# Kernel tuning notes

Hardware: AMD Instinct MI355X
Metric: run time of the kernel (lower is better)

The kernel has to match this reference:

```python
import jax, jax.numpy as jnp
import numpy as np

N = 50000
E = 800000
NUM_GRAPHS = 64
D_IN = 261
D_SAGE = 64
D_LIN = 32
N_SAGE_REST = 6
N_LIN_REST = 3
EPS = 1e-5


def _layernorm(x, g, b):
    mu = jnp.mean(x, axis=-1, keepdims=True)
    var = jnp.mean((x - mu) ** 2, axis=-1, keepdims=True)
    return (x - mu) * jax.lax.rsqrt(var + EPS) * g + b


def _sage_block(x, Wl, bl, Wr, g, b, src, dst, inv_deg, residual):
    # mean aggregation of neighbor (source) features onto targets
    msum = jax.ops.segment_sum(x[src], dst, num_segments=N)  # [N, d]
    mean = msum * inv_deg  # [N, d]
    f = mean @ Wl + bl + x @ Wr  # lin_l(aggr) + lin_r(x); lin_r has no bias
    f = jax.nn.gelu(f, approximate=False)
    f = _layernorm(f, g, b)
    if residual:
        f = f + x
    return f


def _lin_block(x, W, b, g, beta, residual):
    f = jax.nn.gelu(x @ W + b, approximate=False)
    f = _layernorm(f, g, beta)
    if residual:
        f = f + x
    return f


def setup_inputs() -> dict:
    key = jax.random.key(0)
    ks = jax.random.split(key, 24)
    x = jax.random.normal(ks[0], (N, D_IN), dtype=jnp.float32)
    edge_index = jax.random.randint(ks[1], (2, E), 0, N, dtype=jnp.int64)
    batch = jnp.sort(jax.random.randint(ks[2], (N,), 0, NUM_GRAPHS, dtype=jnp.int64))

    def glorot(k, shape):
        fan_in = shape[0]
        return jax.random.normal(k, shape, dtype=jnp.float32) / np.sqrt(fan_in)

    inp = {
        "x": x, "edge_index": edge_index, "batch": batch,
        # first SAGE block (261 -> 64, no residual)
        "Wl0": glorot(ks[3], (D_IN, D_SAGE)), "bl0": jnp.zeros((D_SAGE,), jnp.float32),
        "Wr0": glorot(ks[4], (D_IN, D_SAGE)),
        "g0": jnp.ones((D_SAGE,), jnp.float32), "beta0": jnp.zeros((D_SAGE,), jnp.float32),
        # 6 residual SAGE blocks (64 -> 64), stacked
        "Wl": glorot(ks[5], (N_SAGE_REST, D_SAGE, D_SAGE)),
        "bl": jnp.zeros((N_SAGE_REST, D_SAGE), jnp.float32),
        "Wr": glorot(ks[6], (N_SAGE_REST, D_SAGE, D_SAGE)),
        "g": jnp.ones((N_SAGE_REST, D_SAGE), jnp.float32),
        "beta": jnp.zeros((N_SAGE_REST, D_SAGE), jnp.float32),
        # MLP: first LinearBlock 64 -> 32 (no residual)
        "M0": glorot(ks[7], (D_SAGE, D_LIN)), "mb0": jnp.zeros((D_LIN,), jnp.float32),
        "mg0": jnp.ones((D_LIN,), jnp.float32), "mbeta0": jnp.zeros((D_LIN,), jnp.float32),
        # 3 residual LinearBlocks 32 -> 32, stacked
        "M": glorot(ks[8], (N_LIN_REST, D_LIN, D_LIN)),
        "mb": jnp.zeros((N_LIN_REST, D_LIN), jnp.float32),
        "mg": jnp.ones((N_LIN_REST, D_LIN), jnp.float32),
        "mbeta": jnp.zeros((N_LIN_REST, D_LIN), jnp.float32),
        # final Linear 32 -> 1
        "Wf": glorot(ks[9], (D_LIN, 1)), "bf": jnp.zeros((1,), jnp.float32),
    }
    return inp


def reference(x, edge_index, batch, Wl0, bl0, Wr0, g0, beta0, Wl, bl, Wr, g, beta,
              M0, mb0, mg0, mbeta0, M, mb, mg, mbeta, Wf, bf):
    src, dst = edge_index[0], edge_index[1]
    deg = jax.ops.segment_sum(jnp.ones((E,), x.dtype), dst, num_segments=N)
    inv_deg = (1.0 / jnp.maximum(deg, 1.0))[:, None]  # [N,1]

    h = _sage_block(x, Wl0, bl0, Wr0, g0, beta0, src, dst, inv_deg, residual=False)
    for i in range(N_SAGE_REST):
        h = _sage_block(h, Wl[i], bl[i], Wr[i], g[i], beta[i], src, dst, inv_deg, residual=True)

    pooled = jax.ops.segment_sum(h, batch, num_segments=NUM_GRAPHS)  # [G, 64]

    m = _lin_block(pooled, M0, mb0, mg0, mbeta0, residual=False)
    for i in range(N_LIN_REST):
        m = _lin_block(m, M[i], mb[i], mg[i], mbeta[i], residual=True)
    return m @ Wf + bf  # [G, 1]
```

## Files before the change

### kernel.cpp

```cpp
#include <hip/hip_runtime.h>
#include <hip/hip_bf16.h>
#include <math.h>

#define N_NODES 50000
#define N_EDGES 800000
#define NUM_GRAPHS 64
#define NPAD 50048
#define KPAD0 288
#define PSPLIT 16
#define MAXDEG 64

#define G0_GRID    (NPAD / 32)
#define LAYER_GRID (NPAD / 32)
#define PREPW_TOT  (128 * KPAD0 + 6 * 128 * 64)
#define PREPW_GRID ((PREPW_TOT + 255) / 256)
#define CONV_GRID  (NPAD * (KPAD0 / 8) / 256)

#define SLICES 8
#define NPS 6250
#define SCHUNK 2048
#define SCHUNKS ((N_EDGES + SCHUNK - 1) / SCHUNK)
#define SCAT_GRID (SCHUNKS * SLICES)
#define FRONT_GRID (SCAT_GRID + CONV_GRID + PREPW_GRID)

typedef __attribute__((ext_vector_type(8))) short short8;
typedef __attribute__((ext_vector_type(4))) float f32x4;

__device__ __forceinline__ float gelu_f(float v) {
    return 0.5f * v * (1.0f + erff(v * 0.70710678118654752440f));
}

__device__ __forceinline__ float half_sum32(float v) {
    v += __shfl_xor(v, 1); v += __shfl_xor(v, 2); v += __shfl_xor(v, 4);
    v += __shfl_xor(v, 8); v += __shfl_xor(v, 16);
    return v;
}

__device__ __forceinline__ float group_sum8(float v) {
    v += __shfl_xor(v, 1); v += __shfl_xor(v, 2); v += __shfl_xor(v, 4);
    return v;
}

__device__ __forceinline__ unsigned short f2bf(float f) {
    unsigned int u = __float_as_uint(f);
    unsigned int r = (u + 0x7fffu + ((u >> 16) & 1u)) >> 16;
    return (unsigned short)r;
}

__device__ __forceinline__ float bf_lo(unsigned int u) {
    return __uint_as_float(u << 16);
}
__device__ __forceinline__ float bf_hi(unsigned int u) {
    return __uint_as_float(u & 0xffff0000u);
}


__global__ __launch_bounds__(256) void k_front(
        const int* __restrict__ src, const int* __restrict__ dst,
        int* __restrict__ deg, unsigned short* __restrict__ col64,
        const float* __restrict__ X, unsigned short* __restrict__ Xbf,
        const float* __restrict__ Wl0, const float* __restrict__ Wr0,
        const float* __restrict__ Wl, const float* __restrict__ Wr,
        unsigned short* __restrict__ Bt0, unsigned short* __restrict__ BtR) {
    const int blk = blockIdx.x;
    const int tid = threadIdx.x;
    if (blk < SCAT_GRID) {
        const int s = blk & (SLICES - 1);
        const int c = blk >> 3;
        const int base = c * SCHUNK;
        const int lim = min(base + SCHUNK, N_EDGES);
        for (int i = base + tid; i < lim; i += 256) {
            int d = dst[i];
            if (d / NPS == s) {
                int sv = src[i];
                int pos = atomicAdd(&deg[d], 1);
                if (pos < MAXDEG) col64[(d << 6) + pos] = (unsigned short)sv;
            }
        }
        return;
    }
    if (blk < SCAT_GRID + CONV_GRID) {
        int t = (blk - SCAT_GRID) * 256 + tid;
        int node = t / (KPAD0 / 8);
        int k8 = (t - node * (KPAD0 / 8)) * 8;
        short8 v8;
        if (node < N_NODES) {
            #pragma unroll
            for (int j = 0; j < 8; ++j) {
                int k = k8 + j;
                float val = (k < 261) ? X[(size_t)node * 261 + k] : 0.0f;
                v8[j] = (short)f2bf(val);
            }
        } else {
            #pragma unroll
            for (int j = 0; j < 8; ++j) v8[j] = 0;
        }
        *(short8*)&Xbf[(size_t)node * KPAD0 + k8] = v8;
        return;
    }
    int idx = (blk - SCAT_GRID - CONV_GRID) * 256 + tid;
    const int n0 = 128 * KPAD0;
    if (idx < n0) {
        int j = idx / KPAD0, k = idx - j * KPAD0;
        float v = 0.0f;
        if (k < 261) v = (j < 64) ? Wl0[k * 64 + j] : Wr0[k * 64 + (j - 64)];
        Bt0[idx] = f2bf(v);
    } else if (idx < PREPW_TOT) {
        int r = idx - n0;
        int l = r >> 13;
        int rr = r & 8191;
        int j = rr >> 6, k = rr & 63;
        float v = (j < 64) ? Wl[l * 4096 + k * 64 + j] : Wr[l * 4096 + k * 64 + (j - 64)];
        BtR[r] = f2bf(v);
    }
}


__global__ __launch_bounds__(256) void k_gemm0(
        const unsigned short* __restrict__ Xbf, const unsigned short* __restrict__ Bt0,
        unsigned short* __restrict__ U, float* __restrict__ V) {
    __shared__ __align__(16) unsigned short sB[64 * 296];
    const int tid = threadIdx.x;
    const int lane = tid & 63, wid = tid >> 6;
    const int l16 = lane & 15, quad = lane >> 4;
    const int ch = blockIdx.x & 1;
    const int m0 = (blockIdx.x >> 1) * 64;
    #pragma unroll
    for (int k = 0; k < 9; ++k) {
        int g = k * 256 + tid;
        int row = g / 36;
        int part = (g - row * 36) * 8;
        *(short8*)&sB[row * 296 + part] =
            *(const short8*)&Bt0[(size_t)(ch * 64 + row) * KPAD0 + part];
    }
    f32x4 acc[4];
    #pragma unroll
    for (int j = 0; j < 4; ++j) { acc[j][0] = 0.f; acc[j][1] = 0.f; acc[j][2] = 0.f; acc[j][3] = 0.f; }
    const unsigned short* xr = Xbf + (size_t)(m0 + wid * 16 + l16) * KPAD0 + quad * 8;
    __syncthreads();
    for (int kc = 0; kc < KPAD0; kc += 32) {
        short8 af = *(const short8*)(xr + kc);
        #pragma unroll
        for (int j = 0; j < 4; ++j) {
            short8 bfv = *(const short8*)&sB[(j * 16 + l16) * 296 + kc + quad * 8];
            acc[j] = __builtin_amdgcn_mfma_f32_16x16x32_bf16(af, bfv, acc[j], 0, 0, 0);
        }
    }
    const int rbase = m0 + wid * 16 + quad * 4;
    if (ch == 0) {
        #pragma unroll
        for (int j = 0; j < 4; ++j)
            #pragma unroll
            for (int r = 0; r < 4; ++r)
                U[(size_t)(rbase + r) * 64 + j * 16 + l16] = f2bf(acc[j][r]);
    } else {
        #pragma unroll
        for (int j = 0; j < 4; ++j)
            #pragma unroll
            for (int r = 0; r < 4; ++r)
                V[(size_t)(rbase + r) * 64 + j * 16 + l16] = acc[j][r];
    }
}


__global__ __launch_bounds__(256) void k_layer(
        const unsigned short* __restrict__ U_in, const float* __restrict__ V_in,
        unsigned short* __restrict__ h,
        const int* __restrict__ deg, const unsigned short* __restrict__ col64,
        const float* __restrict__ bias, const float* __restrict__ gam,
        const float* __restrict__ bet,
        const unsigned short* __restrict__ Bt_next,
        unsigned short* __restrict__ U_out, float* __restrict__ V_out,
        const int* __restrict__ batch, float* __restrict__ pool_part,
        int residual, int have_gemm) {
    __shared__ __align__(16) unsigned short sA[2 * 32 * 32];
    __shared__ __align__(16) unsigned short sB[128 * 72];
    const int tid = threadIdx.x;
    const int lane = tid & 63, wid = tid >> 6;
    const int sub = lane >> 3, hl = lane & 7;
    const int base = lane & 56;
    const int m0 = blockIdx.x * 32;
    const uint4* __restrict__ Up = (const uint4*)U_in;

    if (have_gemm) {
        #pragma unroll
        for (int k = 0; k < 4; ++k) {
            int g = k * 256 + tid;
            int row = g >> 3, part = (g & 7) * 8;
            *(short8*)&sB[row * 72 + part] = *(const short8*)&Bt_next[(size_t)row * 64 + part];
        }
    }

    const int nl = wid * 8 + sub;
    const int node = m0 + nl;
    const bool valid = (node < N_NODES);
    const int nd = valid ? node : 0;
    const int dg = valid ? deg[nd] : 0;
    const int cnt = min(dg, MAXDEG);
    uint4 cv = make_uint4(0u, 0u, 0u, 0u);
    if (valid) cv = *(const uint4*)&col64[((size_t)nd << 6) + hl * 8];
    float s0 = 0.f, s1 = 0.f, s2 = 0.f, s3 = 0.f, s4 = 0.f, s5 = 0.f, s6 = 0.f, s7 = 0.f;
    for (int b = 0; b * 8 < cnt; b += 2) {
        #pragma unroll
        for (int hh = 0; hh < 2; ++hh) {
            const int sl = base + b + hh;
            unsigned int p0 = (unsigned int)__shfl((int)cv.x, sl);
            unsigned int p1 = (unsigned int)__shfl((int)cv.y, sl);
            unsigned int p2 = (unsigned int)__shfl((int)cv.z, sl);
            unsigned int p3 = (unsigned int)__shfl((int)cv.w, sl);
            const int eb = (b + hh) * 8;
            int c[8];
            c[0] = (int)(p0 & 0xffffu); c[1] = (int)(p0 >> 16);
            c[2] = (int)(p1 & 0xffffu); c[3] = (int)(p1 >> 16);
            c[4] = (int)(p2 & 0xffffu); c[5] = (int)(p2 >> 16);
            c[6] = (int)(p3 & 0xffffu); c[7] = (int)(p3 >> 16);
            #pragma unroll
            for (int i = 0; i < 8; ++i) {
                uint4 u = (eb + i < cnt) ? Up[(size_t)c[i] * 8 + hl] : make_uint4(0u, 0u, 0u, 0u);
                s0 += bf_lo(u.x); s1 += bf_hi(u.x);
                s2 += bf_lo(u.y); s3 += bf_hi(u.y);
                s4 += bf_lo(u.z); s5 += bf_hi(u.z);
                s6 += bf_lo(u.w); s7 += bf_hi(u.w);
            }
        }
    }
    const float id = 1.0f / fmaxf((float)dg, 1.0f);
    const float4 b0 = *(const float4*)&bias[8 * hl];
    const float4 b1 = *(const float4*)&bias[8 * hl + 4];
    float4 v0 = make_float4(0.f, 0.f, 0.f, 0.f), v1 = v0;
    if (valid) {
        v0 = *(const float4*)&V_in[(size_t)nd * 64 + 8 * hl];
        v1 = *(const float4*)&V_in[(size_t)nd * 64 + 8 * hl + 4];
    }
    float f0 = gelu_f(s0 * id + b0.x + v0.x);
    float f1 = gelu_f(s1 * id + b0.y + v0.y);
    float f2 = gelu_f(s2 * id + b0.z + v0.z);
    float f3 = gelu_f(s3 * id + b0.w + v0.w);
    float f4 = gelu_f(s4 * id + b1.x + v1.x);
    float f5 = gelu_f(s5 * id + b1.y + v1.y);
    float f6 = gelu_f(s6 * id + b1.z + v1.z);
    float f7 = gelu_f(s7 * id + b1.w + v1.w);
    float mu = group_sum8(((f0 + f1) + (f2 + f3)) + ((f4 + f5) + (f6 + f7))) * 0.015625f;
    float d0 = f0 - mu, d1 = f1 - mu, d2 = f2 - mu, d3 = f3 - mu;
    float d4 = f4 - mu, d5 = f5 - mu, d6 = f6 - mu, d7 = f7 - mu;
    float var = group_sum8(((d0 * d0 + d1 * d1) + (d2 * d2 + d3 * d3)) +
                           ((d4 * d4 + d5 * d5) + (d6 * d6 + d7 * d7))) * 0.015625f;
    float rs = rsqrtf(var + 1e-5f);
    const float4 g0v = *(const float4*)&gam[8 * hl];
    const float4 g1v = *(const float4*)&gam[8 * hl + 4];
    const float4 e0v = *(const float4*)&bet[8 * hl];
    const float4 e1v = *(const float4*)&bet[8 * hl + 4];
    f0 = d0 * rs * g0v.x + e0v.x;
    f1 = d1 * rs * g0v.y + e0v.y;
    f2 = d2 * rs * g0v.z + e0v.z;
    f3 = d3 * rs * g0v.w + e0v.w;
    f4 = d4 * rs * g1v.x + e1v.x;
    f5 = d5 * rs * g1v.y + e1v.y;
    f6 = d6 * rs * g1v.z + e1v.z;
    f7 = d7 * rs * g1v.w + e1v.w;
    if (residual && valid) {
        uint4 hu = ((const uint4*)h)[(size_t)nd * 8 + hl];
        f0 += bf_lo(hu.x); f1 += bf_hi(hu.x);
        f2 += bf_lo(hu.y); f3 += bf_hi(hu.y);
        f4 += bf_lo(hu.z); f5 += bf_hi(hu.z);
        f6 += bf_lo(hu.w); f7 += bf_hi(hu.w);
    }

    if (pool_part) {
        const int myg = valid ? batch[nd] : -1;
        const int i_lo = (m0 < N_NODES) ? m0 : (N_NODES - 1);
        const int i_hi = (m0 + 31 < N_NODES) ? (m0 + 31) : (N_NODES - 1);
        const int g_lo = batch[i_lo];
        const int g_hi = batch[i_hi];
        const int split = blockIdx.x & (PSPLIT - 1);
        for (int g = g_lo; g <= g_hi; ++g) {
            const bool mine = (myg == g);
            float p0 = mine ? f0 : 0.f, p1 = mine ? f1 : 0.f;
            float p2 = mine ? f2 : 0.f, p3 = mine ? f3 : 0.f;
            float p4 = mine ? f4 : 0.f, p5 = mine ? f5 : 0.f;
            float p6 = mine ? f6 : 0.f, p7 = mine ? f7 : 0.f;
            p0 += __shfl_xor(p0, 8);  p1 += __shfl_xor(p1, 8);
            p2 += __shfl_xor(p2, 8);  p3 += __shfl_xor(p3, 8);
            p4 += __shfl_xor(p4, 8);  p5 += __shfl_xor(p5, 8);
            p6 += __shfl_xor(p6, 8);  p7 += __shfl_xor(p7, 8);
            p0 += __shfl_xor(p0, 16); p1 += __shfl_xor(p1, 16);
            p2 += __shfl_xor(p2, 16); p3 += __shfl_xor(p3, 16);
            p4 += __shfl_xor(p4, 16); p5 += __shfl_xor(p5, 16);
            p6 += __shfl_xor(p6, 16); p7 += __shfl_xor(p7, 16);
            p0 += __shfl_xor(p0, 32); p1 += __shfl_xor(p1, 32);
            p2 += __shfl_xor(p2, 32); p3 += __shfl_xor(p3, 32);
            p4 += __shfl_xor(p4, 32); p5 += __shfl_xor(p5, 32);
            p6 += __shfl_xor(p6, 32); p7 += __shfl_xor(p7, 32);
            if (sub == 0) {
                float* dp = &pool_part[((size_t)g * PSPLIT + split) * 64 + 8 * hl];
                atomicAdd(dp + 0, p0); atomicAdd(dp + 1, p1);
                atomicAdd(dp + 2, p2); atomicAdd(dp + 3, p3);
                atomicAdd(dp + 4, p4); atomicAdd(dp + 5, p5);
                atomicAdd(dp + 6, p6); atomicAdd(dp + 7, p7);
            }
        }
        return;
    }

    uint4 outw;
    outw.x = (unsigned int)f2bf(f0) | ((unsigned int)f2bf(f1) << 16);
    outw.y = (unsigned int)f2bf(f2) | ((unsigned int)f2bf(f3) << 16);
    outw.z = (unsigned int)f2bf(f4) | ((unsigned int)f2bf(f5) << 16);
    outw.w = (unsigned int)f2bf(f6) | ((unsigned int)f2bf(f7) << 16);
    if (valid) ((uint4*)h)[(size_t)nd * 8 + hl] = outw;
    *(uint4*)&sA[(((hl >> 2) * 32 + nl) << 5) + (hl & 3) * 8] = outw;

    if (!have_gemm) return;
    __syncthreads();

    const int l16 = lane & 15, quad = lane >> 4;
    const int wrow = wid & 1, colh = wid >> 1;
    f32x4 acc[4];
    #pragma unroll
    for (int j = 0; j < 4; ++j) { acc[j][0] = 0.f; acc[j][1] = 0.f; acc[j][2] = 0.f; acc[j][3] = 0.f; }
    #pragma unroll
    for (int kc = 0; kc < 64; kc += 32) {
        short8 af = *(const short8*)&sA[(((kc >> 5) * 32 + wrow * 16 + l16) << 5) + quad * 8];
        #pragma unroll
        for (int j = 0; j < 4; ++j) {
            short8 bfv = *(const short8*)&sB[(colh * 64 + j * 16 + l16) * 72 + kc + quad * 8];
            acc[j] = __builtin_amdgcn_mfma_f32_16x16x32_bf16(af, bfv, acc[j], 0, 0, 0);
        }
    }
    const int rbase = m0 + wrow * 16 + quad * 4;
    if (colh == 0) {
        #pragma unroll
        for (int j = 0; j < 4; ++j)
            #pragma unroll
            for (int r = 0; r < 4; ++r)
                U_out[(size_t)(rbase + r) * 64 + j * 16 + l16] = f2bf(acc[j][r]);
    } else {
        #pragma unroll
        for (int j = 0; j < 4; ++j)
            #pragma unroll
            for (int r = 0; r < 4; ++r)
                V_out[(size_t)(rbase + r) * 64 + j * 16 + l16] = acc[j][r];
    }
}


__global__ __launch_bounds__(1024) void k_head(const float* __restrict__ partial,
                                               const float* __restrict__ M0, const float* __restrict__ mb0,
                                               const float* __restrict__ mg0, const float* __restrict__ mbeta0,
                                               const float* __restrict__ M, const float* __restrict__ mb,
                                               const float* __restrict__ mg, const float* __restrict__ mbeta,
                                               const float* __restrict__ Wf, const float* __restrict__ bf,
                                               float* __restrict__ out) {
    __shared__ float sP[64 * 64];
    __shared__ float sA[64 * 33];
    __shared__ float sB[64 * 33];
    const int tx = threadIdx.x, ty = threadIdx.y;
    const int tid = ty * 32 + tx;
    for (int i = tid; i < 64 * 64; i += 1024) {
        int g = i >> 6, f = i & 63;
        float s = 0.0f;
        #pragma unroll
        for (int s2 = 0; s2 < PSPLIT; ++s2) s += partial[(size_t)(g * PSPLIT + s2) * 64 + f];
        sP[i] = s;
    }
    __syncthreads();
    #pragma unroll
    for (int rr = 0; rr < 2; ++rr) {
        int r = ty + rr * 32;
        float a = mb0[tx];
        for (int k = 0; k < 64; ++k) a += sP[r * 64 + k] * M0[k * 32 + tx];
        a = gelu_f(a);
        float mu = half_sum32(a) * (1.0f / 32.0f);
        float d = a - mu;
        float var = half_sum32(d * d) * (1.0f / 32.0f);
        a = d * rsqrtf(var + 1e-5f) * mg0[tx] + mbeta0[tx];
        sA[r * 33 + tx] = a;
    }
    __syncthreads();
    float* cur = sA;
    float* nxt = sB;
    for (int L = 0; L < 3; ++L) {
        const float* Mi = M + L * 32 * 32;
        const float* mbi = mb + L * 32;
        const float* mgi = mg + L * 32;
        const float* mbetai = mbeta + L * 32;
        #pragma unroll
        for (int rr = 0; rr < 2; ++rr) {
            int r = ty + rr * 32;
            float a = mbi[tx];
            for (int k = 0; k < 32; ++k) a += cur[r * 33 + k] * Mi[k * 32 + tx];
            a = gelu_f(a);
            float mu = half_sum32(a) * (1.0f / 32.0f);
            float d = a - mu;
            float var = half_sum32(d * d) * (1.0f / 32.0f);
            a = d * rsqrtf(var + 1e-5f) * mgi[tx] + mbetai[tx] + cur[r * 33 + tx];
            nxt[r * 33 + tx] = a;
        }
        __syncthreads();
        float* t = cur; cur = nxt; nxt = t;
    }
    #pragma unroll
    for (int rr = 0; rr < 2; ++rr) {
        int r = ty + rr * 32;
        float p = cur[r * 33 + tx] * Wf[tx];
        p = half_sum32(p);
        if (tx == 0) out[r] = p + bf[0];
    }
}


extern "C" void kernel_launch(void* const* d_in, const int* in_sizes, int n_in,
                              void* d_out, int out_size, void* d_ws, size_t ws_size,
                              hipStream_t stream) {
    const int N = N_NODES;
    const int E = N_EDGES;

    const float* x    = (const float*)d_in[0];
    const int* eidx   = (const int*)d_in[1];
    const int* batch  = (const int*)d_in[2];
    const float* Wl0  = (const float*)d_in[3];
    const float* bl0  = (const float*)d_in[4];
    const float* Wr0  = (const float*)d_in[5];
    const float* g0   = (const float*)d_in[6];
    const float* bet0 = (const float*)d_in[7];
    const float* Wl   = (const float*)d_in[8];
    const float* bl   = (const float*)d_in[9];
    const float* Wr   = (const float*)d_in[10];
    const float* gR   = (const float*)d_in[11];
    const float* betR = (const float*)d_in[12];
    const float* M0   = (const float*)d_in[13];
    const float* mb0  = (const float*)d_in[14];
    const float* mg0  = (const float*)d_in[15];
    const float* mbe0 = (const float*)d_in[16];
    const float* M    = (const float*)d_in[17];
    const float* mb   = (const float*)d_in[18];
    const float* mg   = (const float*)d_in[19];
    const float* mbe  = (const float*)d_in[20];
    const float* Wf   = (const float*)d_in[21];
    const float* bf   = (const float*)d_in[22];

    const int* src = eidx;
    const int* dst = eidx + E;

    char* p = (char*)d_ws;
    auto alloc = [&](size_t bytes) -> void* {
        void* q = (void*)p;
        p += (bytes + 255) & ~(size_t)255;
        return q;
    };
    int*   deg     = (int*)alloc((size_t)N * 4);
    float* partial = (float*)alloc((size_t)NUM_GRAPHS * PSPLIT * 64 * 4);
    unsigned short* col64 = (unsigned short*)alloc((size_t)N * MAXDEG * 2);
    unsigned short* Bt0 = (unsigned short*)alloc((size_t)128 * KPAD0 * 2);
    unsigned short* BtR = (unsigned short*)alloc((size_t)6 * 128 * 64 * 2);
    unsigned short* Xbf = (unsigned short*)alloc((size_t)NPAD * KPAD0 * 2);
    unsigned short* Ua  = (unsigned short*)alloc((size_t)NPAD * 64 * 2);
    unsigned short* Ub  = (unsigned short*)alloc((size_t)NPAD * 64 * 2);
    float* Va   = (float*)alloc((size_t)NPAD * 64 * 4);
    float* Vb   = (float*)alloc((size_t)NPAD * 64 * 4);
    unsigned short* hbuf = (unsigned short*)alloc((size_t)NPAD * 64 * 2);

    size_t zspan = (size_t)((char*)col64 - (char*)deg);
    hipMemsetAsync(deg, 0, zspan, stream);

    k_front<<<FRONT_GRID, 256, 0, stream>>>(
        src, dst, deg, col64, x, Xbf, Wl0, Wr0, Wl, Wr, Bt0, BtR);

    k_gemm0<<<G0_GRID, 256, 0, stream>>>(Xbf, Bt0, Ua, Va);

    unsigned short* Uin = Ua;  float* Vin = Va;
    unsigned short* Uout = Ub; float* Vout = Vb;
    for (int i = 0; i < 7; ++i) {
        const float* bias = (i == 0) ? bl0  : bl  + (size_t)(i - 1) * 64;
        const float* gam  = (i == 0) ? g0   : gR  + (size_t)(i - 1) * 64;
        const float* bet  = (i == 0) ? bet0 : betR + (size_t)(i - 1) * 64;
        const int have_gemm = (i < 6);
        float* pool_part = (i == 6) ? partial : nullptr;
        k_layer<<<LAYER_GRID, 256, 0, stream>>>(
            Uin, Vin, hbuf, deg, col64, bias, gam, bet,
            have_gemm ? (BtR + (size_t)i * 128 * 64) : BtR,
            Uout, Vout, batch, pool_part, (i > 0) ? 1 : 0, have_gemm);
        unsigned short* tu = Uin; Uin = Uout; Uout = tu;
        float* tv = Vin; Vin = Vout; Vout = tv;
    }

    k_head<<<1, dim3(32, 32), 0, stream>>>(partial, M0, mb0, mg0, mbe0, M, mb, mg, mbe, Wf, bf, (float*)d_out);
}
```

Before: 381.9 us.

## Co-schedule edge scatter with first-layer GEMM in an interleaved kernel

Moves the edge-to-CSR scatter out of the front prep kernel and interleaves its blocks with the first GEMM blocks inside one kernel (two scatter blocks per GEMM block), launched as two halves. The aim is to overlap the atomic-heavy, latency-bound scatter with the compute-bound MFMA GEMM so both share the GPU. It also adds nontemporal loads on X, src and dst to reduce cache pollution. This adds one more kernel launch and makes the scatter depend on finishing the conversion kernel first. The GEMM is still correct, since the prep kernel that produces Xbf runs beforehand.

```diff
diff --git a/kernel.cpp b/kernel.cpp
--- a/kernel.cpp
+++ b/kernel.cpp
@@ -10,18 +10,21 @@
 #define PSPLIT 16
 #define MAXDEG 64
 
-#define G0_GRID    (NPAD / 32)
 #define LAYER_GRID (NPAD / 32)
 #define PREPW_TOT  (128 * KPAD0 + 6 * 128 * 64)
 #define PREPW_GRID ((PREPW_TOT + 255) / 256)
 #define CONV_GRID  (NPAD * (KPAD0 / 8) / 256)
+#define PREP2_GRID (CONV_GRID + PREPW_GRID)
 
 #define SLICES 8
 #define NPS 6250
 #define SCHUNK 2048
 #define SCHUNKS ((N_EDGES + SCHUNK - 1) / SCHUNK)
 #define SCAT_GRID (SCHUNKS * SLICES)
-#define FRONT_GRID (SCAT_GRID + CONV_GRID + PREPW_GRID)
+
+#define MID_TRIPLES 1564
+#define MID_GRID (MID_TRIPLES * 3)
+#define MID_HALF (MID_GRID / 2)
 
 typedef __attribute__((ext_vector_type(8))) short short8;
 typedef __attribute__((ext_vector_type(4))) float f32x4;
@@ -55,32 +58,15 @@
 }
 
 
-__global__ __launch_bounds__(256) void k_front(
-        const int* __restrict__ src, const int* __restrict__ dst,
-        int* __restrict__ deg, unsigned short* __restrict__ col64,
+__global__ __launch_bounds__(256) void k_prep2(
         const float* __restrict__ X, unsigned short* __restrict__ Xbf,
         const float* __restrict__ Wl0, const float* __restrict__ Wr0,
         const float* __restrict__ Wl, const float* __restrict__ Wr,
         unsigned short* __restrict__ Bt0, unsigned short* __restrict__ BtR) {
     const int blk = blockIdx.x;
     const int tid = threadIdx.x;
-    if (blk < SCAT_GRID) {
-        const int s = blk & (SLICES - 1);
-        const int c = blk >> 3;
-        const int base = c * SCHUNK;
-        const int lim = min(base + SCHUNK, N_EDGES);
-        for (int i = base + tid; i < lim; i += 256) {
-            int d = dst[i];
-            if (d / NPS == s) {
-                int sv = src[i];
-                int pos = atomicAdd(&deg[d], 1);
-                if (pos < MAXDEG) col64[(d << 6) + pos] = (unsigned short)sv;
-            }
-        }
-        return;
-    }
-    if (blk < SCAT_GRID + CONV_GRID) {
-        int t = (blk - SCAT_GRID) * 256 + tid;
+    if (blk < CONV_GRID) {
+        int t = blk * 256 + tid;
         int node = t / (KPAD0 / 8);
         int k8 = (t - node * (KPAD0 / 8)) * 8;
         short8 v8;
@@ -88,7 +74,7 @@
             #pragma unroll
             for (int j = 0; j < 8; ++j) {
                 int k = k8 + j;
-                float val = (k < 261) ? X[(size_t)node * 261 + k] : 0.0f;
+                float val = (k < 261) ? __builtin_nontemporal_load(&X[(size_t)node * 261 + k]) : 0.0f;
                 v8[j] = (short)f2bf(val);
             }
         } else {
@@ -98,7 +84,7 @@
         *(short8*)&Xbf[(size_t)node * KPAD0 + k8] = v8;
         return;
     }
-    int idx = (blk - SCAT_GRID - CONV_GRID) * 256 + tid;
+    int idx = (blk - CONV_GRID) * 256 + tid;
     const int n0 = 128 * KPAD0;
     if (idx < n0) {
         int j = idx / KPAD0, k = idx - j * KPAD0;
@@ -116,20 +102,42 @@
 }
 
 
-__global__ __launch_bounds__(256) void k_gemm0(
+__global__ __launch_bounds__(256) void k_mid(
+        int offset,
+        const int* __restrict__ src, const int* __restrict__ dst,
+        int* __restrict__ deg, unsigned short* __restrict__ col64,
         const unsigned short* __restrict__ Xbf, const unsigned short* __restrict__ Bt0,
         unsigned short* __restrict__ U, float* __restrict__ V) {
     __shared__ __align__(16) unsigned short sB[64 * 296];
+    const int blk = blockIdx.x + offset;
     const int tid = threadIdx.x;
+    const int g = blk / 3;
+    const int r = blk - g * 3;
+    if (r < 2) {
+        const int sid = g * 2 + r;
+        const int s = sid & (SLICES - 1);
+        const int c = sid >> 3;
+        const int base = c * SCHUNK;
+        const int lim = min(base + SCHUNK, N_EDGES);
+        for (int i = base + tid; i < lim; i += 256) {
+            int d = __builtin_nontemporal_load(&dst[i]);
+            if (d / NPS == s) {
+                int sv = __builtin_nontemporal_load(&src[i]);
+                int pos = atomicAdd(&deg[d], 1);
+                if (pos < MAXDEG) col64[(d << 6) + pos] = (unsigned short)sv;
+            }
+        }
+        return;
+    }
     const int lane = tid & 63, wid = tid >> 6;
     const int l16 = lane & 15, quad = lane >> 4;
-    const int ch = blockIdx.x & 1;
-    const int m0 = (blockIdx.x >> 1) * 64;
+    const int ch = g & 1;
+    const int m0 = (g >> 1) * 64;
     #pragma unroll
     for (int k = 0; k < 9; ++k) {
-        int g = k * 256 + tid;
-        int row = g / 36;
-        int part = (g - row * 36) * 8;
+        int gg = k * 256 + tid;
+        int row = gg / 36;
+        int part = (gg - row * 36) * 8;
         *(short8*)&sB[row * 296 + part] =
             *(const short8*)&Bt0[(size_t)(ch * 64 + row) * KPAD0 + part];
     }
@@ -151,14 +159,14 @@
         #pragma unroll
         for (int j = 0; j < 4; ++j)
             #pragma unroll
-            for (int r = 0; r < 4; ++r)
-                U[(size_t)(rbase + r) * 64 + j * 16 + l16] = f2bf(acc[j][r]);
+            for (int rr2 = 0; rr2 < 4; ++rr2)
+                U[(size_t)(rbase + rr2) * 64 + j * 16 + l16] = f2bf(acc[j][rr2]);
     } else {
         #pragma unroll
         for (int j = 0; j < 4; ++j)
             #pragma unroll
-            for (int r = 0; r < 4; ++r)
-                V[(size_t)(rbase + r) * 64 + j * 16 + l16] = acc[j][r];
+            for (int rr2 = 0; rr2 < 4; ++rr2)
+                V[(size_t)(rbase + rr2) * 64 + j * 16 + l16] = acc[j][rr2];
     }
 }
 
@@ -463,10 +471,10 @@
     size_t zspan = (size_t)((char*)col64 - (char*)deg);
     hipMemsetAsync(deg, 0, zspan, stream);
 
-    k_front<<<FRONT_GRID, 256, 0, stream>>>(
-        src, dst, deg, col64, x, Xbf, Wl0, Wr0, Wl, Wr, Bt0, BtR);
-
-    k_gemm0<<<G0_GRID, 256, 0, stream>>>(Xbf, Bt0, Ua, Va);
+    k_prep2<<<PREP2_GRID, 256, 0, stream>>>(x, Xbf, Wl0, Wr0, Wl, Wr, Bt0, BtR);
+
+    k_mid<<<MID_HALF, 256, 0, stream>>>(0, src, dst, deg, col64, Xbf, Bt0, Ua, Va);
+    k_mid<<<MID_HALF, 256, 0, stream>>>(MID_HALF, src, dst, deg, col64, Xbf, Bt0, Ua, Va);
 
     unsigned short* Uin = Ua;  float* Vin = Va;
     unsigned short* Uout = Ub; float* Vout = Vb;
```

Result: slower. 436.1 us (+14.2%).

## Split front kernel into prep and two scatter launches, nontemporal loads, hoist loads

Applied to the files above, without the earlier changes.

Splits the fused front kernel into a separate X/weight conversion kernel and an edge-scatter kernel. The scatter is launched as two halves, and dst/src/X reads now use nontemporal loads. In the layer kernel, the V_in and residual h loads are moved ahead of the neighbor-gather loop so their latency overlaps with the gather. The extra launches add overhead, and the streaming-load hints may or may not help the atomic scatter.

```diff
diff --git a/kernel.cpp b/kernel.cpp
--- a/kernel.cpp
+++ b/kernel.cpp
@@ -15,13 +15,13 @@
 #define PREPW_TOT  (128 * KPAD0 + 6 * 128 * 64)
 #define PREPW_GRID ((PREPW_TOT + 255) / 256)
 #define CONV_GRID  (NPAD * (KPAD0 / 8) / 256)
+#define PREP2_GRID (CONV_GRID + PREPW_GRID)
 
 #define SLICES 8
 #define NPS 6250
 #define SCHUNK 2048
 #define SCHUNKS ((N_EDGES + SCHUNK - 1) / SCHUNK)
-#define SCAT_GRID (SCHUNKS * SLICES)
-#define FRONT_GRID (SCAT_GRID + CONV_GRID + PREPW_GRID)
+#define SCAT_SPLIT 196
 
 typedef __attribute__((ext_vector_type(8))) short short8;
 typedef __attribute__((ext_vector_type(4))) float f32x4;
@@ -55,32 +55,15 @@
 }
 
 
-__global__ __launch_bounds__(256) void k_front(
-        const int* __restrict__ src, const int* __restrict__ dst,
-        int* __restrict__ deg, unsigned short* __restrict__ col64,
+__global__ __launch_bounds__(256) void k_prep2(
         const float* __restrict__ X, unsigned short* __restrict__ Xbf,
         const float* __restrict__ Wl0, const float* __restrict__ Wr0,
         const float* __restrict__ Wl, const float* __restrict__ Wr,
         unsigned short* __restrict__ Bt0, unsigned short* __restrict__ BtR) {
     const int blk = blockIdx.x;
     const int tid = threadIdx.x;
-    if (blk < SCAT_GRID) {
-        const int s = blk & (SLICES - 1);
-        const int c = blk >> 3;
-        const int base = c * SCHUNK;
-        const int lim = min(base + SCHUNK, N_EDGES);
-        for (int i = base + tid; i < lim; i += 256) {
-            int d = dst[i];
-            if (d / NPS == s) {
-                int sv = src[i];
-                int pos = atomicAdd(&deg[d], 1);
-                if (pos < MAXDEG) col64[(d << 6) + pos] = (unsigned short)sv;
-            }
-        }
-        return;
-    }
-    if (blk < SCAT_GRID + CONV_GRID) {
-        int t = (blk - SCAT_GRID) * 256 + tid;
+    if (blk < CONV_GRID) {
+        int t = blk * 256 + tid;
         int node = t / (KPAD0 / 8);
         int k8 = (t - node * (KPAD0 / 8)) * 8;
         short8 v8;
@@ -88,7 +71,7 @@
             #pragma unroll
             for (int j = 0; j < 8; ++j) {
                 int k = k8 + j;
-                float val = (k < 261) ? X[(size_t)node * 261 + k] : 0.0f;
+                float val = (k < 261) ? __builtin_nontemporal_load(&X[(size_t)node * 261 + k]) : 0.0f;
                 v8[j] = (short)f2bf(val);
             }
         } else {
@@ -98,7 +81,7 @@
         *(short8*)&Xbf[(size_t)node * KPAD0 + k8] = v8;
         return;
     }
-    int idx = (blk - SCAT_GRID - CONV_GRID) * 256 + tid;
+    int idx = (blk - CONV_GRID) * 256 + tid;
     const int n0 = 128 * KPAD0;
     if (idx < n0) {
         int j = idx / KPAD0, k = idx - j * KPAD0;
@@ -112,6 +95,26 @@
         int j = rr >> 6, k = rr & 63;
         float v = (j < 64) ? Wl[l * 4096 + k * 64 + j] : Wr[l * 4096 + k * 64 + (j - 64)];
         BtR[r] = f2bf(v);
+    }
+}
+
+
+__global__ __launch_bounds__(256) void k_scat(
+        int cbase,
+        const int* __restrict__ src, const int* __restrict__ dst,
+        int* __restrict__ deg, unsigned short* __restrict__ col64) {
+    const int sid = cbase * 8 + blockIdx.x;
+    const int s = sid & (SLICES - 1);
+    const int c = sid >> 3;
+    const int base = c * SCHUNK;
+    const int lim = min(base + SCHUNK, N_EDGES);
+    for (int i = base + (int)threadIdx.x; i < lim; i += 256) {
+        int d = __builtin_nontemporal_load(&dst[i]);
+        if (d / NPS == s) {
+            int sv = __builtin_nontemporal_load(&src[i]);
+            int pos = atomicAdd(&deg[d], 1);
+            if (pos < MAXDEG) col64[(d << 6) + pos] = (unsigned short)sv;
+        }
     }
 }
 
@@ -199,6 +202,15 @@
     const int cnt = min(dg, MAXDEG);
     uint4 cv = make_uint4(0u, 0u, 0u, 0u);
     if (valid) cv = *(const uint4*)&col64[((size_t)nd << 6) + hl * 8];
+
+    float4 v0 = make_float4(0.f, 0.f, 0.f, 0.f), v1 = v0;
+    if (valid) {
+        v0 = *(const float4*)&V_in[(size_t)nd * 64 + 8 * hl];
+        v1 = *(const float4*)&V_in[(size_t)nd * 64 + 8 * hl + 4];
+    }
+    uint4 hu = make_uint4(0u, 0u, 0u, 0u);
+    if (residual && valid) hu = ((const uint4*)h)[(size_t)nd * 8 + hl];
+
     float s0 = 0.f, s1 = 0.f, s2 = 0.f, s3 = 0.f, s4 = 0.f, s5 = 0.f, s6 = 0.f, s7 = 0.f;
     for (int b = 0; b * 8 < cnt; b += 2) {
         #pragma unroll
@@ -227,11 +239,6 @@
     const float id = 1.0f / fmaxf((float)dg, 1.0f);
     const float4 b0 = *(const float4*)&bias[8 * hl];
     const float4 b1 = *(const float4*)&bias[8 * hl + 4];
-    float4 v0 = make_float4(0.f, 0.f, 0.f, 0.f), v1 = v0;
-    if (valid) {
-        v0 = *(const float4*)&V_in[(size_t)nd * 64 + 8 * hl];
-        v1 = *(const float4*)&V_in[(size_t)nd * 64 + 8 * hl + 4];
-    }
     float f0 = gelu_f(s0 * id + b0.x + v0.x);
     float f1 = gelu_f(s1 * id + b0.y + v0.y);
     float f2 = gelu_f(s2 * id + b0.z + v0.z);
@@ -259,7 +266,6 @@
     f6 = d6 * rs * g1v.z + e1v.z;
     f7 = d7 * rs * g1v.w + e1v.w;
     if (residual && valid) {
-        uint4 hu = ((const uint4*)h)[(size_t)nd * 8 + hl];
         f0 += bf_lo(hu.x); f1 += bf_hi(hu.x);
         f2 += bf_lo(hu.y); f3 += bf_hi(hu.y);
         f4 += bf_lo(hu.z); f5 += bf_hi(hu.z);
@@ -463,8 +469,10 @@
     size_t zspan = (size_t)((char*)col64 - (char*)deg);
     hipMemsetAsync(deg, 0, zspan, stream);
 
-    k_front<<<FRONT_GRID, 256, 0, stream>>>(
-        src, dst, deg, col64, x, Xbf, Wl0, Wr0, Wl, Wr, Bt0, BtR);
+    k_prep2<<<PREP2_GRID, 256, 0, stream>>>(x, Xbf, Wl0, Wr0, Wl, Wr, Bt0, BtR);
+
+    k_scat<<<SCAT_SPLIT * 8, 256, 0, stream>>>(0, src, dst, deg, col64);
+    k_scat<<<(SCHUNKS - SCAT_SPLIT) * 8, 256, 0, stream>>>(SCAT_SPLIT, src, dst, deg, col64);
 
     k_gemm0<<<G0_GRID, 256, 0, stream>>>(Xbf, Bt0, Ua, Va);
 
```

New measurement: 415.7 us. 8.9% more time.
